# Optimization experiments

Measured on AMD Instinct MI355X. Metric: run time of the kernel, lower is better.

The kernel has to match this reference:

```python
import jax, jax.numpy as jnp
import numpy as np

EPS = 1e-5

def conv(x, w, stride=1, pad=0, groups=1):
    # x: NCHW, w: OIHW
    return jax.lax.conv_general_dilated(
        x, w, window_strides=(stride, stride),
        padding=[(pad, pad), (pad, pad)],
        dimension_numbers=("NCHW", "OIHW", "NCHW"),
        feature_group_count=groups)

def bn_eval(x, gamma, beta, mean, var):
    scale = (gamma / jnp.sqrt(var + EPS))[None, :, None, None]
    shift = (beta - mean * gamma / jnp.sqrt(var + EPS))[None, :, None, None]
    return x * scale + shift

def setup_inputs() -> dict:
    key = jax.random.key(0)
    ks = jax.random.split(key, 12)
    B, Cin, H, W = 32, 64, 56, 56
    hidden, red, Cout, K = 384, 16, 64, 3
    f32 = jnp.float32
    x = jax.random.normal(ks[0], (B, Cin, H, W), dtype=f32)
    w_exp = jax.random.normal(ks[1], (hidden, Cin, 3, 3), dtype=f32) * 0.05
    w_dw  = jax.random.normal(ks[2], (hidden, 1, K, K), dtype=f32) * 0.1
    w_se1 = jax.random.normal(ks[3], (red, hidden, 1, 1), dtype=f32) * 0.05
    w_se2 = jax.random.normal(ks[4], (hidden, red, 1, 1), dtype=f32) * 0.1
    w_pw  = jax.random.normal(ks[5], (Cout, hidden, 1, 1), dtype=f32) * 0.05
    def bn_params(k, c):
        k1, k2 = jax.random.split(k)
        return (jnp.ones((c,), f32), jnp.zeros((c,), f32),
                jax.random.normal(k1, (c,), dtype=f32) * 0.01,
                jax.random.uniform(k2, (c,), dtype=f32, minval=0.5, maxval=1.5))
    g1, b1, m1, v1 = bn_params(ks[6], hidden)
    g2, b2, m2, v2 = bn_params(ks[7], hidden)
    g3, b3, m3, v3 = bn_params(ks[8], Cout)
    return dict(x=x, w_exp=w_exp, g1=g1, b1=b1, m1=m1, v1=v1,
                w_dw=w_dw, g2=g2, b2=b2, m2=m2, v2=v2,
                w_se1=w_se1, w_se2=w_se2, w_pw=w_pw,
                g3=g3, b3=b3, m3=m3, v3=v3)

def reference(x, w_exp, g1, b1, m1, v1, w_dw, g2, b2, m2, v2,
              w_se1, w_se2, w_pw, g3, b3, m3, v3):
    hidden = w_exp.shape[0]
    # expand conv (3x3) + BN + SiLU
    h = jax.nn.silu(bn_eval(conv(x, w_exp, stride=1, pad=1), g1, b1, m1, v1))
    # depthwise conv + BN + SiLU
    d = jax.nn.silu(bn_eval(conv(h, w_dw, stride=1, pad=1, groups=hidden), g2, b2, m2, v2))
    # squeeze-excitation: global avg pool -> 1x1 -> SiLU -> 1x1 -> sigmoid -> scale
    s = jnp.mean(d, axis=(2, 3), keepdims=True)            # [B, hidden, 1, 1]
    s = jax.nn.silu(conv(s, w_se1))
    s = jax.nn.sigmoid(conv(s, w_se2))
    d = d * s
    # pointwise projection + BN
    y = bn_eval(conv(d, w_pw), g3, b3, m3, v3)
    # eval mode: stochastic_depth is identity; quant_skip == (identity-quantized) input
    return y + x
```

## Files before the change

### kernel.cpp

```cpp
#include <hip/hip_runtime.h>

typedef unsigned short u16;
typedef unsigned int u32;
typedef __attribute__((ext_vector_type(2))) u32 u32x2;
typedef __attribute__((ext_vector_type(4))) u32 u32x4;
typedef __attribute__((ext_vector_type(2))) float f32x2;
typedef __attribute__((ext_vector_type(4))) float f32x4;
typedef __attribute__((ext_vector_type(8))) short s16x8;

#define DEV __device__ __forceinline__

DEV float bflo(u32 u){ union{u32 i; float f;} c; c.i = u << 16; return c.f; }
DEV float bfhi(u32 u){ union{u32 i; float f;} c; c.i = u & 0xffff0000u; return c.f; }
DEV u16 f2b(float f){
  union{float f; u32 u;} c; c.f = f;
  u32 u = c.u;
  u32 r = (u + 0x7fffu + ((u >> 16) & 1u)) >> 16;
  return (u16)r;
}
DEV float fsilu(float v){ return v / (1.f + __expf(-v)); }

typedef const __attribute__((address_space(1))) u32 gu32;
typedef __attribute__((address_space(3))) u32 lu32;
DEV void gload16(const u32* g, u32* l) {
  __builtin_amdgcn_global_load_lds((gu32*)g, (lu32*)l, 16, 0, 0);
}

constexpr int Bn = 32, Cin = 64, H = 56, Wd = 56, HID = 384, CO = 64;
constexpr int HW = H * Wd;
constexpr float EPS = 1e-5f;

constexpr int WTAP = 128 * 64;
constexpr int WOCT = 9 * WTAP;
constexpr int XTROW = 64 * 64;
constexpr int PWP = 392;

__global__ __launch_bounds__(256) void k_prep_wbn(
    const float* __restrict__ w,
    const float* __restrict__ g1, const float* __restrict__ b1,
    const float* __restrict__ m1, const float* __restrict__ v1,
    const float* __restrict__ g3, const float* __restrict__ b3,
    const float* __restrict__ m3, const float* __restrict__ v3,
    u16* __restrict__ wt,
    float* __restrict__ sc1, float* __restrict__ sh1,
    float* __restrict__ sc3, float* __restrict__ sh3)
{
  const int blk = blockIdx.x;
  if (blk < 864) {
    int t = blk * 256 + threadIdx.x;
    int octile = t / WOCT, r = t - octile * WOCT;
    int tap = r / WTAP, r2 = r - tap * WTAP;
    int ocl = r2 >> 6, col = r2 & 63;
    int physo = col >> 3, j = col & 7;
    int olog = physo ^ (ocl & 7);
    int ic = olog * 8 + j;
    int oc = octile * 128 + ocl;
    wt[t] = f2b(w[(oc * Cin + ic) * 9 + tap]);
  } else {
    for (int t = threadIdx.x; t < HID; t += 256) {
      float sc = g1[t] * rsqrtf(v1[t] + EPS);
      sc1[t] = sc;
      sh1[t] = b1[t] - m1[t] * sc;
    }
    if (threadIdx.x < CO) {
      int t = threadIdx.x;
      float sc = g3[t] * rsqrtf(v3[t] + EPS);
      sc3[t] = sc;
      sh3[t] = b3[t] - m3[t] * sc;
    }
  }
}

__global__ __launch_bounds__(256) void k_prep_x(
    const float* __restrict__ x, u16* __restrict__ xt, int b0)
{
  const int row = blockIdx.x;
  const int b = blockIdx.y, gb = b0 + b;
  const int tid = threadIdx.x;
  u16* dst = xt + ((size_t)b * 58 + row) * XTROW;
  if (row == 0 || row == 57) {
    for (int i = tid; i < 2048; i += 256) ((u32*)dst)[i] = 0;
    return;
  }
  const int y = row - 1;
  __shared__ u16 sx[64 * 58];
  {
    const int ic = tid >> 2, seg = tid & 3;
    const float* xp = x + ((size_t)(gb * Cin + ic) * H + y) * Wd + seg * 14;
    #pragma unroll
    for (int t = 0; t < 14; ++t) sx[ic * 58 + seg * 14 + t] = f2b(xp[t]);
  }
  __syncthreads();
  #pragma unroll
  for (int it = 0; it < 16; ++it) {
    const int slot = it * 4 + (tid >> 6);
    const int j = tid & 63;
    u16 v = 0;
    if (slot >= 1 && slot <= 56) {
      int ic = (((j >> 3) ^ (slot & 7)) << 3) | (j & 7);
      v = sx[ic * 58 + (slot - 1)];
    }
    dst[slot * 64 + j] = v;
  }
}

__global__ __launch_bounds__(256, 2) void k_expand_mfma(
    const u16* __restrict__ xt, const u16* __restrict__ wt,
    const float* __restrict__ sc1, const float* __restrict__ sh1,
    u16* __restrict__ h, int b0)
{
  (void)b0;
  __shared__ u16 sB[6 * XTROW];
  __shared__ u16 sA[2][WTAP];
  const int tid = threadIdx.x;
  const int yq = blockIdx.x, b = blockIdx.y;
  const int y0 = yq * 4;
  const int wave = tid >> 6, ln = tid & 63;
  const int lane15 = ln & 15, quad = ln >> 4;

  {
    const u32* xsrc = (const u32*)(xt + ((size_t)b * 58 + y0) * XTROW);
    #pragma unroll
    for (int it = 0; it < 12; ++it) {
      int chunk = it * 256 + tid;
      gload16(xsrc + chunk * 4, (u32*)sB + (chunk & ~63) * 4);
    }
    const u32* wsrc = (const u32*)wt;
    #pragma unroll
    for (int it = 0; it < 4; ++it) {
      int chunk = it * 256 + tid;
      gload16(wsrc + chunk * 4, (u32*)sA[0] + (chunk & ~63) * 4);
    }
  }
  __syncthreads();

  const int y = y0 + wave;

  for (int octile = 0; octile < 3; ++octile) {
    f32x4 acc[8][4];
    #pragma unroll
    for (int ms = 0; ms < 8; ++ms)
      #pragma unroll
      for (int ns = 0; ns < 4; ++ns) acc[ms][ns] = (f32x4){0.f, 0.f, 0.f, 0.f};

    #pragma unroll
    for (int tap = 0; tap < 9; ++tap) {
      const int step = octile * 9 + tap;
      const int buf = (octile + tap) & 1;
      const bool pre = (step < 26);

      u32x4 pf0, pf1, pf2, pf3;
      if (pre) {
        const u16* wnx = wt + (size_t)(step + 1) * WTAP;
        pf0 = *(const u32x4*)&wnx[(0 * 256 + tid) * 8];
        pf1 = *(const u32x4*)&wnx[(1 * 256 + tid) * 8];
        pf2 = *(const u32x4*)&wnx[(2 * 256 + tid) * 8];
        pf3 = *(const u32x4*)&wnx[(3 * 256 + tid) * 8];
      }

      constexpr int dyv[9] = {0,0,0,1,1,1,2,2,2};
      constexpr int dxv[9] = {0,1,2,0,1,2,0,1,2};
      const int dy = dyv[tap], dx = dxv[tap];
      const u16* sAc = sA[buf];
      __builtin_amdgcn_s_setprio(1);
      #pragma unroll
      for (int kk = 0; kk < 2; ++kk) {
        s16x8 bf[4];
        #pragma unroll
        for (int ns = 0; ns < 4; ++ns) {
          int row = wave + dy;
          int slot = ns * 16 + lane15 + dx;
          int po = (kk * 4 + quad) ^ (slot & 7);
          bf[ns] = *(const s16x8*)&sB[(row * 64 + slot) * 64 + po * 8];
        }
        #pragma unroll
        for (int ms = 0; ms < 8; ++ms) {
          int ocl = ms * 16 + lane15;
          int po = (kk * 4 + quad) ^ (ocl & 7);
          s16x8 af = *(const s16x8*)&sAc[ocl * 64 + po * 8];
          #pragma unroll
          for (int ns = 0; ns < 4; ++ns)
            acc[ms][ns] = __builtin_amdgcn_mfma_f32_16x16x32_bf16(
                af, bf[ns], acc[ms][ns], 0, 0, 0);
        }
      }
      __builtin_amdgcn_s_setprio(0);

      if (pre) {
        u16* sAn = sA[buf ^ 1];
        *(u32x4*)&sAn[(0 * 256 + tid) * 8] = pf0;
        *(u32x4*)&sAn[(1 * 256 + tid) * 8] = pf1;
        *(u32x4*)&sAn[(2 * 256 + tid) * 8] = pf2;
        *(u32x4*)&sAn[(3 * 256 + tid) * 8] = pf3;
      }
      __syncthreads();
    }

    #pragma unroll
    for (int ms = 0; ms < 8; ++ms) {
      int oc0 = octile * 128 + ms * 16 + quad * 4;
      f32x4 sc = *(const f32x4*)&sc1[oc0];
      f32x4 sh = *(const f32x4*)&sh1[oc0];
      float scr[4] = {sc.x, sc.y, sc.z, sc.w};
      float shr[4] = {sh.x, sh.y, sh.z, sh.w};
      #pragma unroll
      for (int ns = 0; ns < 4; ++ns) {
        int xg = ns * 16 + lane15;
        if (xg < Wd) {
          float av[4] = {acc[ms][ns].x, acc[ms][ns].y, acc[ms][ns].z, acc[ms][ns].w};
          #pragma unroll
          for (int r = 0; r < 4; ++r) {
            float val = fsilu(av[r] * scr[r] + shr[r]);
            h[((size_t)(b * HID + oc0 + r) * H + y) * Wd + xg] = f2b(val);
          }
        }
      }
    }
  }
}

__global__ __launch_bounds__(256) void k_dw(
    const u16* __restrict__ h, const float* __restrict__ wdw,
    const float* __restrict__ g2, const float* __restrict__ b2,
    const float* __restrict__ m2, const float* __restrict__ v2,
    u16* __restrict__ d, float* __restrict__ mean)
{
  __shared__ u32 sdw[1568];
  __shared__ float red[4];
  const int tid = threadIdx.x;
  const int c = blockIdx.x, b = blockIdx.y;
  const u32* hp32 = (const u32*)(h + (size_t)(b * HID + c) * HW);

  gload16(hp32 + tid * 4, sdw + (tid & ~63) * 4);
  if (tid < 136) {
    int chunk = 256 + tid;
    gload16(hp32 + chunk * 4, sdw + (chunk & ~63) * 4);
  }

  f32x2 wv2[9];
  #pragma unroll
  for (int t = 0; t < 9; ++t) {
    float w = wdw[c * 9 + t];
    wv2[t] = (f32x2){w, w};
  }
  const float sc = g2[c] * rsqrtf(v2[c] + EPS);
  const float sh = b2[c] - m2[c] * sc;
  const f32x2 scv = (f32x2){sc, sc}, shv = (f32x2){sh, sh};

  __syncthreads();

  float lsum = 0.f;
  if (tid < 224) {
    const int r7 = tid / 28;
    const int wd = tid - r7 * 28;
    const int r0 = r7 * 7;
    u32* dp32 = (u32*)(d + (size_t)(b * HID + c) * HW);

    auto loadrow = [&](int rr, f32x2* P) {
      u32 m = 0, c0 = 0, p = 0;
      if (rr >= 0 && rr < 56) {
        const u32* rp = sdw + rr * 28;
        c0 = rp[wd];
        if (wd > 0)  m = rp[wd - 1];
        if (wd < 27) p = rp[wd + 1];
      }
      float f_hm = bfhi(m), f_lc = bflo(c0), f_hc = bfhi(c0), f_lp = bflo(p);
      P[0] = (f32x2){f_hm, f_lc};
      P[1] = (f32x2){f_lc, f_hc};
      P[2] = (f32x2){f_hc, f_lp};
    };

    f32x2 Pa[3], Pb[3], Pc[3];
    loadrow(r0 - 1, Pa);
    loadrow(r0,     Pb);
    f32x2 ls2 = (f32x2){0.f, 0.f};
    #pragma unroll
    for (int i = 0; i < 7; ++i) {
      loadrow(r0 + i + 1, Pc);
      f32x2 s = (f32x2){0.f, 0.f};
      #pragma unroll
      for (int dx = 0; dx < 3; ++dx) s = __builtin_elementwise_fma(Pa[dx], wv2[dx], s);
      #pragma unroll
      for (int dx = 0; dx < 3; ++dx) s = __builtin_elementwise_fma(Pb[dx], wv2[3 + dx], s);
      #pragma unroll
      for (int dx = 0; dx < 3; ++dx) s = __builtin_elementwise_fma(Pc[dx], wv2[6 + dx], s);
      f32x2 t = __builtin_elementwise_fma(s, scv, shv);
      f32x2 val;
      val.x = fsilu(t.x);
      val.y = fsilu(t.y);
      ls2 += val;
      u32 pk;
      asm("v_cvt_pk_bf16_f32 %0, %1, %2" : "=v"(pk) : "v"(val.x), "v"(val.y));
      dp32[(r0 + i) * 28 + wd] = pk;
      #pragma unroll
      for (int q = 0; q < 3; ++q) { Pa[q] = Pb[q]; Pb[q] = Pc[q]; }
    }
    lsum = ls2.x + ls2.y;
  }

  #pragma unroll
  for (int off = 32; off > 0; off >>= 1) lsum += __shfl_down(lsum, off);
  if ((tid & 63) == 0) red[tid >> 6] = lsum;
  __syncthreads();
  if (tid == 0)
    mean[b * HID + c] = (red[0] + red[1] + red[2] + red[3]) * (1.f / 3136.f);
}

__global__ __launch_bounds__(256) void k_se_fold(
    const float* __restrict__ mean, const float* __restrict__ w1,
    const float* __restrict__ w2, const float* __restrict__ wpw,
    const float* __restrict__ sc3, u16* __restrict__ apk)
{
  __shared__ float smn[HID];
  __shared__ float sps[16 * 17];
  __shared__ float ss1[16];
  __shared__ float ssf[HID];
  const int b = blockIdx.x, tid = threadIdx.x;
  for (int c = tid; c < HID; c += 256) smn[c] = mean[b * HID + c];
  __syncthreads();
  {
    int r = tid >> 4, j = tid & 15;
    float p = 0.f;
    for (int c = j; c < HID; c += 16) p += smn[c] * w1[r * HID + c];
    sps[r * 17 + j] = p;
  }
  __syncthreads();
  if (tid < 16) {
    float s = 0.f;
    #pragma unroll
    for (int q = 0; q < 16; ++q) s += sps[tid * 17 + q];
    ss1[tid] = fsilu(s);
  }
  __syncthreads();
  for (int c = tid; c < HID; c += 256) {
    float s = 0.f;
    #pragma unroll
    for (int q = 0; q < 16; ++q) s += ss1[q] * w2[c * 16 + q];
    ssf[c] = 1.f / (1.f + __expf(-s));
  }
  __syncthreads();
  u16* ap = apk + (size_t)b * CO * PWP;
  for (int i = tid; i < 6144; i += 256) {
    int e = i * 4, co = e / 384, k = e - co * 384;
    f32x4 wv = *(const f32x4*)&wpw[e];
    f32x4 sf = *(const f32x4*)&ssf[k];
    float s3 = sc3[co];
    u32x2 pk;
    pk.x = (u32)f2b(wv.x * sf.x * s3) | ((u32)f2b(wv.y * sf.y * s3) << 16);
    pk.y = (u32)f2b(wv.z * sf.z * s3) | ((u32)f2b(wv.w * sf.w * s3) << 16);
    *(u32x2*)&ap[co * PWP + k] = pk;
  }
}

__global__ __launch_bounds__(256, 2) void k_pw_mfma(
    const u16* __restrict__ d, const u16* __restrict__ apk,
    const float* __restrict__ sh3,
    const float* __restrict__ x, float* __restrict__ out, int b0)
{
  __shared__ u16 sAw[64 * PWP];
  __shared__ u32 dtw[4 * 1024];
  const int tid = threadIdx.x;
  const int b = blockIdx.y, gb = b0 + b;
  const int p0 = blockIdx.x * 256;
  const int wave = tid >> 6, ln = tid & 63;
  const int lane15 = ln & 15, quad = ln >> 4;

  {
    const u32* ap = (const u32*)(apk + (size_t)b * CO * PWP);
    #pragma unroll
    for (int i = 0; i < 13; ++i) {
      int chunk = i * 256 + tid;
      if (chunk < 3136)
        gload16(ap + chunk * 4, (u32*)sAw + (chunk & ~63) * 4);
    }
  }
  __syncthreads();

  f32x4 acc[4][4];
  #pragma unroll
  for (int ms = 0; ms < 4; ++ms)
    #pragma unroll
    for (int ns = 0; ns < 4; ++ns) acc[ms][ns] = (f32x4){0.f, 0.f, 0.f, 0.f};

  const int cpair8 = ln >> 3;
  const int pxo = (ln & 7) * 8;
  const int swz = ln & 3;
  const int pbase = p0 + wave * 64;
  u32* mydt = &dtw[wave * 1024];
  const bool ld_ok = (pbase + pxo + 8 <= HW);
  const u16* dbase = d + (size_t)b * HID * HW + pbase + pxo;

  u32x4 pr0[2], pr1[2];
  #pragma unroll
  for (int ci = 0; ci < 2; ++ci) {
    pr0[ci] = (u32x4){0,0,0,0}; pr1[ci] = (u32x4){0,0,0,0};
    if (ld_ok) {
      int c = 2 * (ci * 8 + cpair8);
      const u16* dpp = dbase + (size_t)c * HW;
      pr0[ci] = *(const u32x4*)dpp;
      pr1[ci] = *(const u32x4*)(dpp + HW);
    }
  }

  for (int ks = 0; ks < 12; ++ks) {
    #pragma unroll
    for (int ci = 0; ci < 2; ++ci) {
      int k4 = ci * 2 + (cpair8 >> 2);
      u32* w0 = &mydt[pxo * 16 + ((k4 ^ swz) << 2) + (cpair8 & 3)];
      u32x4 r0 = pr0[ci], r1 = pr1[ci];
      w0[0 * 16] = (r0.x & 0xffffu) | (r1.x << 16);
      w0[1 * 16] = (r0.x >> 16)     | (r1.x & 0xffff0000u);
      w0[2 * 16] = (r0.y & 0xffffu) | (r1.y << 16);
      w0[3 * 16] = (r0.y >> 16)     | (r1.y & 0xffff0000u);
      w0[4 * 16] = (r0.z & 0xffffu) | (r1.z << 16);
      w0[5 * 16] = (r0.z >> 16)     | (r1.z & 0xffff0000u);
      w0[6 * 16] = (r0.w & 0xffffu) | (r1.w << 16);
      w0[7 * 16] = (r0.w >> 16)     | (r1.w & 0xffff0000u);
    }
    if (ks < 11) {
      #pragma unroll
      for (int ci = 0; ci < 2; ++ci) {
        if (ld_ok) {
          int c = (ks + 1) * 32 + 2 * (ci * 8 + cpair8);
          const u16* dpp = dbase + (size_t)c * HW;
          pr0[ci] = *(const u32x4*)dpp;
          pr1[ci] = *(const u32x4*)(dpp + HW);
        }
      }
    }
    const int k0 = ks * 32;
    s16x8 af[4], bf[4];
    #pragma unroll
    for (int ms = 0; ms < 4; ++ms) {
      int ocl = ms * 16 + lane15;
      af[ms] = *(const s16x8*)&sAw[ocl * PWP + k0 + quad * 8];
    }
    #pragma unroll
    for (int ns = 0; ns < 4; ++ns) {
      int pxl = ns * 16 + lane15;
      int p4 = quad ^ ((pxl >> 3) & 3);
      bf[ns] = *(const s16x8*)((const u16*)mydt + pxl * 32 + p4 * 8);
    }
    #pragma unroll
    for (int ms = 0; ms < 4; ++ms)
      #pragma unroll
      for (int ns = 0; ns < 4; ++ns)
        acc[ms][ns] = __builtin_amdgcn_mfma_f32_16x16x32_bf16(
            af[ms], bf[ns], acc[ms][ns], 0, 0, 0);
  }

  #pragma unroll
  for (int ns = 0; ns < 4; ++ns) {
    int p = pbase + ns * 16 + lane15;
    if (p < HW) {
      #pragma unroll
      for (int ms = 0; ms < 4; ++ms) {
        int co0 = ms * 16 + quad * 4;
        float av[4] = {acc[ms][ns].x, acc[ms][ns].y, acc[ms][ns].z, acc[ms][ns].w};
        #pragma unroll
        for (int r = 0; r < 4; ++r) {
          size_t idx = (size_t)(gb * CO + co0 + r) * HW + p;
          out[idx] = av[r] + sh3[co0 + r] + x[idx];
        }
      }
    }
  }
}

extern "C" void kernel_launch(void* const* d_in, const int* in_sizes, int n_in,
                              void* d_out, int out_size, void* d_ws, size_t ws_size,
                              hipStream_t stream)
{
  (void)in_sizes; (void)n_in; (void)out_size;
  const float* x     = (const float*)d_in[0];
  const float* w_exp = (const float*)d_in[1];
  const float* g1 = (const float*)d_in[2];
  const float* b1 = (const float*)d_in[3];
  const float* m1 = (const float*)d_in[4];
  const float* v1 = (const float*)d_in[5];
  const float* w_dw = (const float*)d_in[6];
  const float* g2 = (const float*)d_in[7];
  const float* b2 = (const float*)d_in[8];
  const float* m2 = (const float*)d_in[9];
  const float* v2 = (const float*)d_in[10];
  const float* w_se1 = (const float*)d_in[11];
  const float* w_se2 = (const float*)d_in[12];
  const float* w_pw  = (const float*)d_in[13];
  const float* g3 = (const float*)d_in[14];
  const float* b3 = (const float*)d_in[15];
  const float* m3 = (const float*)d_in[16];
  const float* v3 = (const float*)d_in[17];

  const size_t perB = (size_t)HID * HW * 2 * 2 + HID * 4
                    + (size_t)58 * XTROW * 2 + (size_t)CO * PWP * 2;
  const size_t fixed = 221184 * 2 + HID * 8 + CO * 8;
  int bc = Bn;
  while (bc > 1 && fixed + (size_t)bc * perB > ws_size) bc >>= 1;

  u16* wt = (u16*)d_ws;
  float* sc1 = (float*)(wt + 221184);
  float* sh1 = sc1 + HID;
  float* sc3 = sh1 + HID;
  float* sh3 = sc3 + CO;
  u16* h  = (u16*)(sh3 + CO);
  u16* dd = h + (size_t)bc * HID * HW;
  float* mean = (float*)(dd + (size_t)bc * HID * HW);
  u16* xt = (u16*)(mean + (size_t)bc * HID);
  u16* apk = xt + (size_t)bc * 58 * XTROW;

  k_prep_wbn<<<865, 256, 0, stream>>>(w_exp, g1, b1, m1, v1, g3, b3, m3, v3,
                                      wt, sc1, sh1, sc3, sh3);

  for (int b0 = 0; b0 < Bn; b0 += bc) {
    k_prep_x<<<dim3(58, bc), 256, 0, stream>>>(x, xt, b0);
    k_expand_mfma<<<dim3(14, bc), 256, 0, stream>>>(xt, wt, sc1, sh1, h, b0);
    k_dw<<<dim3(HID, bc), 256, 0, stream>>>(h, w_dw, g2, b2, m2, v2, dd, mean);
    k_se_fold<<<bc, 256, 0, stream>>>(mean, w_se1, w_se2, w_pw, sc3, apk);
    k_pw_mfma<<<dim3(13, bc), 256, 0, stream>>>(dd, apk, sh3,
                                                x, (float*)d_out, b0);
  }
}
```

Baseline: 251.0 us.

## Compute two output rows per wave in expand conv to reuse weight fragments

Each wave of the expand 3x3 MFMA kernel now computes two output rows instead of one, so a block covers 8 rows and the grid halves. Each weight fragment loaded from LDS is reused across both rows, and the shared input tile grows to 10 rows. This lowers LDS weight traffic and the number of weight restreams per output row, at the cost of doubling accumulator registers (occupancy bound dropped to 1 block per CU) and halving the number of blocks.

Measured after the change: 274.8 us. +9.5%, slower.

```diff
diff --git a/kernel.cpp b/kernel.cpp
--- a/kernel.cpp
+++ b/kernel.cpp
@@ -104,24 +104,24 @@
   }
 }
 
-__global__ __launch_bounds__(256, 2) void k_expand_mfma(
+__global__ __launch_bounds__(256, 1) void k_expand_mfma(
     const u16* __restrict__ xt, const u16* __restrict__ wt,
     const float* __restrict__ sc1, const float* __restrict__ sh1,
     u16* __restrict__ h, int b0)
 {
   (void)b0;
-  __shared__ u16 sB[6 * XTROW];
+  __shared__ u16 sB[10 * XTROW + 128];
   __shared__ u16 sA[2][WTAP];
   const int tid = threadIdx.x;
-  const int yq = blockIdx.x, b = blockIdx.y;
-  const int y0 = yq * 4;
+  const int yo = blockIdx.x, b = blockIdx.y;
+  const int y0 = yo * 8;
   const int wave = tid >> 6, ln = tid & 63;
   const int lane15 = ln & 15, quad = ln >> 4;
 
   {
     const u32* xsrc = (const u32*)(xt + ((size_t)b * 58 + y0) * XTROW);
     #pragma unroll
-    for (int it = 0; it < 12; ++it) {
+    for (int it = 0; it < 20; ++it) {
       int chunk = it * 256 + tid;
       gload16(xsrc + chunk * 4, (u32*)sB + (chunk & ~63) * 4);
     }
@@ -134,14 +134,15 @@
   }
   __syncthreads();
 
-  const int y = y0 + wave;
-
   for (int octile = 0; octile < 3; ++octile) {
-    f32x4 acc[8][4];
+    f32x4 acc[8][4], acc2[8][4];
     #pragma unroll
     for (int ms = 0; ms < 8; ++ms)
       #pragma unroll
-      for (int ns = 0; ns < 4; ++ns) acc[ms][ns] = (f32x4){0.f, 0.f, 0.f, 0.f};
+      for (int ns = 0; ns < 4; ++ns) {
+        acc[ms][ns]  = (f32x4){0.f, 0.f, 0.f, 0.f};
+        acc2[ms][ns] = (f32x4){0.f, 0.f, 0.f, 0.f};
+      }
 
     #pragma unroll
     for (int tap = 0; tap < 9; ++tap) {
@@ -165,24 +166,30 @@
       __builtin_amdgcn_s_setprio(1);
       #pragma unroll
       for (int kk = 0; kk < 2; ++kk) {
-        s16x8 bf[4];
-        #pragma unroll
-        for (int ns = 0; ns < 4; ++ns) {
-          int row = wave + dy;
-          int slot = ns * 16 + lane15 + dx;
-          int po = (kk * 4 + quad) ^ (slot & 7);
-          bf[ns] = *(const s16x8*)&sB[(row * 64 + slot) * 64 + po * 8];
-        }
+        s16x8 af[8], bf0[4], bf1[4];
         #pragma unroll
         for (int ms = 0; ms < 8; ++ms) {
           int ocl = ms * 16 + lane15;
           int po = (kk * 4 + quad) ^ (ocl & 7);
-          s16x8 af = *(const s16x8*)&sAc[ocl * 64 + po * 8];
+          af[ms] = *(const s16x8*)&sAc[ocl * 64 + po * 8];
+        }
+        #pragma unroll
+        for (int ns = 0; ns < 4; ++ns) {
+          int slot = ns * 16 + lane15 + dx;
+          int po = (kk * 4 + quad) ^ (slot & 7);
+          int row0 = 2 * wave + dy;
+          bf0[ns] = *(const s16x8*)&sB[(row0 * 64 + slot) * 64 + po * 8];
+          bf1[ns] = *(const s16x8*)&sB[((row0 + 1) * 64 + slot) * 64 + po * 8];
+        }
+        #pragma unroll
+        for (int ms = 0; ms < 8; ++ms)
           #pragma unroll
-          for (int ns = 0; ns < 4; ++ns)
-            acc[ms][ns] = __builtin_amdgcn_mfma_f32_16x16x32_bf16(
-                af, bf[ns], acc[ms][ns], 0, 0, 0);
-        }
+          for (int ns = 0; ns < 4; ++ns) {
+            acc[ms][ns]  = __builtin_amdgcn_mfma_f32_16x16x32_bf16(
+                af[ms], bf0[ns], acc[ms][ns], 0, 0, 0);
+            acc2[ms][ns] = __builtin_amdgcn_mfma_f32_16x16x32_bf16(
+                af[ms], bf1[ns], acc2[ms][ns], 0, 0, 0);
+          }
       }
       __builtin_amdgcn_s_setprio(0);
 
@@ -207,11 +214,15 @@
       for (int ns = 0; ns < 4; ++ns) {
         int xg = ns * 16 + lane15;
         if (xg < Wd) {
+          const int ya = y0 + 2 * wave;
           float av[4] = {acc[ms][ns].x, acc[ms][ns].y, acc[ms][ns].z, acc[ms][ns].w};
+          float bv[4] = {acc2[ms][ns].x, acc2[ms][ns].y, acc2[ms][ns].z, acc2[ms][ns].w};
           #pragma unroll
           for (int r = 0; r < 4; ++r) {
-            float val = fsilu(av[r] * scr[r] + shr[r]);
-            h[((size_t)(b * HID + oc0 + r) * H + y) * Wd + xg] = f2b(val);
+            float v0 = fsilu(av[r] * scr[r] + shr[r]);
+            float v1 = fsilu(bv[r] * scr[r] + shr[r]);
+            h[((size_t)(b * HID + oc0 + r) * H + ya) * Wd + xg] = f2b(v0);
+            h[((size_t)(b * HID + oc0 + r) * H + ya + 1) * Wd + xg] = f2b(v1);
           }
         }
       }
@@ -513,7 +524,7 @@
 
   for (int b0 = 0; b0 < Bn; b0 += bc) {
     k_prep_x<<<dim3(58, bc), 256, 0, stream>>>(x, xt, b0);
-    k_expand_mfma<<<dim3(14, bc), 256, 0, stream>>>(xt, wt, sc1, sh1, h, b0);
+    k_expand_mfma<<<dim3(7, bc), 256, 0, stream>>>(xt, wt, sc1, sh1, h, b0);
     k_dw<<<dim3(HID, bc), 256, 0, stream>>>(h, w_dw, g2, b2, m2, v2, dd, mean);
     k_se_fold<<<bc, 256, 0, stream>>>(mean, w_se1, w_se2, w_pw, sc3, apk);
     k_pw_mfma<<<dim3(13, bc), 256, 0, stream>>>(dd, apk, sh3,
```
